# Kernel optimization log

Hardware: AMD Instinct MI355X
Metric: run time of the kernel (lower is better)

## Reference

```python
import jax, jax.numpy as jnp
import numpy as np

N = 50000
E = 600000
IN_DIM = 256
OUT_DIM = 128
SCALE = 1.8
K = 2
ALPHA = 0.15
EPS = 1e-12  # matches F.normalize eps


def setup_inputs() -> dict:
    key = jax.random.key(0)
    k1, k2, k3, k4 = jax.random.split(key, 4)
    x = jax.random.normal(k1, (N, IN_DIM), dtype=jnp.float32)
    edge_index = jax.random.randint(k2, (2, E), 0, N, dtype=jnp.int64)
    # nn.Linear params (Kaiming-uniform-ish init scale)
    lim = 1.0 / np.sqrt(IN_DIM)
    W = jax.random.uniform(k3, (OUT_DIM, IN_DIM), dtype=jnp.float32, minval=-lim, maxval=lim)
    b = jax.random.uniform(k4, (OUT_DIM,), dtype=jnp.float32, minval=-lim, maxval=lim)
    return {"x": x, "edge_index": edge_index, "W": W, "b": b}


def _gcn_norm(edge_index, num_nodes):
    # add self loops, symmetric normalization D^-1/2 A D^-1/2
    loops = jnp.arange(num_nodes, dtype=edge_index.dtype)
    row = jnp.concatenate([edge_index[0], loops])  # source
    col = jnp.concatenate([edge_index[1], loops])  # target
    deg = jax.ops.segment_sum(jnp.ones_like(col, dtype=jnp.float32), col,
                              num_segments=num_nodes)
    dinv = jnp.where(deg > 0, jax.lax.rsqrt(deg), 0.0)
    w = dinv[row] * dinv[col]
    return row, col, w


def reference(x, edge_index, W, b):
    # linear
    h = x @ W.T + b  # [N, OUT_DIM]
    # L2 normalize over feature dim, then scale
    nrm = jnp.sqrt(jnp.sum(h * h, axis=1, keepdims=True))
    h = h / jnp.maximum(nrm, EPS) * SCALE
    # APPNP propagation (eval mode: edge dropout disabled)
    row, col, w = _gcn_norm(edge_index, N)
    z = h
    for _ in range(K):
        msg = w[:, None] * z[row]  # gather + weight, [E+N, OUT_DIM]
        agg = jax.ops.segment_sum(msg, col, num_segments=N)
        z = (1.0 - ALPHA) * agg + ALPHA * h
    return z
```

## Files before the change

### kernel.cpp

```cpp
#include <hip/hip_runtime.h>
#include <hip/hip_bf16.h>

#define NNODES 50000
#define IN_DIM 256
#define OUT_DIM 128
#define SCALE 1.8f
#define ALPHA 0.15f
#define DSTRIDE 64
#define GEMM_BLOCKS 782

typedef unsigned short ushort_t;
typedef __attribute__((ext_vector_type(8))) _Float16 f16x8;
typedef __attribute__((ext_vector_type(4))) float f32x4;


__device__ __forceinline__ unsigned short f2bf_rne(float f) {
    unsigned int u = __float_as_uint(f);
    unsigned int r = u + 0x7fffu + ((u >> 16) & 1u);
    return (unsigned short)(r >> 16);
}

__device__ __forceinline__ float2 bf2_to_f2(unsigned int p) {
    float2 f;
    f.x = __uint_as_float(p << 16);
    f.y = __uint_as_float(p & 0xffff0000u);
    return f;
}

__device__ __forceinline__ unsigned int f2_to_bf2(float x, float y) {
    return (unsigned int)f2bf_rne(x) | ((unsigned int)f2bf_rne(y) << 16);
}

__device__ __forceinline__ unsigned short f2h(float f) {
    _Float16 h = (_Float16)f;
    return *(unsigned short*)&h;
}


#define XPAD 264

__global__ void __launch_bounds__(256, 4) prep_gemm_kernel(
        const float* __restrict__ x, const float* __restrict__ W,
        const float* __restrict__ b,
        const int* __restrict__ row, const int* __restrict__ col, int E,
        int* __restrict__ cnt, ushort_t* __restrict__ csr16,
        ushort_t* __restrict__ u0b) {
    __shared__ __align__(16) ushort_t xh[64][XPAD];

    if (blockIdx.x >= GEMM_BLOCKS) {
        int e0 = ((blockIdx.x - GEMM_BLOCKS) * 256 + threadIdx.x) * 2;
        if (e0 < E) {
            int2 rr = *(const int2*)(row + e0);
            int2 cc = *(const int2*)(col + e0);
            int p0 = atomicAdd(&cnt[cc.x], 1);
            if (p0 < DSTRIDE) csr16[(size_t)cc.x * DSTRIDE + p0] = (ushort_t)rr.x;
            int p1 = atomicAdd(&cnt[cc.y], 1);
            if (p1 < DSTRIDE) csr16[(size_t)cc.y * DSTRIDE + p1] = (ushort_t)rr.y;
        }
        return;
    }

    const int t = threadIdx.x;
    const int wv = t >> 6;
    const int lane = t & 63;
    const int q = lane >> 4;
    const int c = lane & 15;
    const int rowBase = blockIdx.x * 64;

    f16x8 wf[2][8];
    float bias[2];
    #pragma unroll
    for (int j = 0; j < 2; ++j) {
        const size_t base = (size_t)((2 * wv + j) * 16 + c) * IN_DIM + q * 8;
        #pragma unroll
        for (int kt = 0; kt < 8; ++kt) {
            float4 w0 = *(const float4*)(W + base + kt * 32);
            float4 w1 = *(const float4*)(W + base + kt * 32 + 4);
            f16x8 wp;
            wp[0] = (_Float16)w0.x; wp[1] = (_Float16)w0.y;
            wp[2] = (_Float16)w0.z; wp[3] = (_Float16)w0.w;
            wp[4] = (_Float16)w1.x; wp[5] = (_Float16)w1.y;
            wp[6] = (_Float16)w1.z; wp[7] = (_Float16)w1.w;
            wf[j][kt] = wp;
        }
        bias[j] = b[(2 * wv + j) * 16 + c];
    }

    #pragma unroll
    for (int it = 0; it < 16; ++it) {
        int s = it * 256 + t;
        int r = s >> 6;
        int ks = (s & 63) * 4;
        int grow = rowBase + r;
        float4 v = make_float4(0.f, 0.f, 0.f, 0.f);
        if (grow < NNODES) v = *(const float4*)(x + (size_t)grow * IN_DIM + ks);
        uint2 p;
        p.x = (unsigned int)f2h(v.x) | ((unsigned int)f2h(v.y) << 16);
        p.y = (unsigned int)f2h(v.z) | ((unsigned int)f2h(v.w) << 16);
        *(uint2*)&xh[r][ks] = p;
    }
    __syncthreads();

    f32x4 acc[4][2];
    #pragma unroll
    for (int m = 0; m < 4; ++m)
        #pragma unroll
        for (int j = 0; j < 2; ++j) {
            acc[m][j][0] = bias[j]; acc[m][j][1] = bias[j];
            acc[m][j][2] = bias[j]; acc[m][j][3] = bias[j];
        }

    #pragma unroll
    for (int kt = 0; kt < 8; ++kt) {
        const int kb = kt * 32 + q * 8;
        #pragma unroll
        for (int m = 0; m < 4; ++m) {
            f16x8 a = *(const f16x8*)&xh[m * 16 + c][kb];
            #pragma unroll
            for (int j = 0; j < 2; ++j)
                acc[m][j] = __builtin_amdgcn_mfma_f32_16x16x32_f16(a, wf[j][kt], acc[m][j], 0, 0, 0);
        }
    }

    float psum[4][4];
    #pragma unroll
    for (int m = 0; m < 4; ++m)
        #pragma unroll
        for (int r = 0; r < 4; ++r)
            psum[m][r] = acc[m][0][r] * acc[m][0][r] + acc[m][1][r] * acc[m][1][r];
    #pragma unroll
    for (int mask = 1; mask < 16; mask <<= 1)
        #pragma unroll
        for (int m = 0; m < 4; ++m)
            #pragma unroll
            for (int r = 0; r < 4; ++r)
                psum[m][r] += __shfl_xor(psum[m][r], mask);

    __syncthreads();
    float* red = (float*)&xh[0][0];
    float* scl = red + 64 * 8;
    if (c == 0) {
        #pragma unroll
        for (int m = 0; m < 4; ++m)
            #pragma unroll
            for (int r = 0; r < 4; ++r)
                red[(m * 16 + q * 4 + r) * 8 + wv] = psum[m][r];
    }
    __syncthreads();
    if (t < 64) {
        float s = red[t * 8 + 0] + red[t * 8 + 1] + red[t * 8 + 2] + red[t * 8 + 3];
        scl[t] = SCALE / fmaxf(sqrtf(s), 1e-12f);
    }
    __syncthreads();

    #pragma unroll
    for (int m = 0; m < 4; ++m) {
        #pragma unroll
        for (int r = 0; r < 4; ++r) {
            int lrow = m * 16 + q * 4 + r;
            int grow = rowBase + lrow;
            if (grow < NNODES) {
                float sc = scl[lrow];
                #pragma unroll
                for (int j = 0; j < 2; ++j) {
                    float o = acc[m][j][r] * sc;
                    u0b[(size_t)grow * OUT_DIM + (2 * wv + j) * 16 + c] = f2bf_rne(o);
                }
            }
        }
    }
}


template <int FINAL>
__global__ void __launch_bounds__(256) gather_kernel(
        const int* __restrict__ cnt, const ushort_t* __restrict__ csr16,
        const unsigned int* __restrict__ sin, const unsigned int* __restrict__ u0,
        unsigned int* __restrict__ sout_b, float* __restrict__ out_f) {
    const int wv = threadIdx.x >> 6;
    const int lane = threadIdx.x & 63;
    const int qd = lane >> 4;
    const int d16 = lane & 15;
    const int c = blockIdx.x * 4 + wv;

    const int deg = cnt[c];
    int n = deg;
    if (n > DSTRIDE) n = DSTRIDE;
    int idx = 0;
    if (lane < n) idx = (int)csr16[(size_t)c * DSTRIDE + lane];

    float2 a[4];
    #pragma unroll
    for (int k = 0; k < 4; ++k) a[k] = make_float2(0.f, 0.f);

    int j = 0;
    for (; j + 8 <= n; j += 8) {
        int r0 = __shfl(idx, j + qd);
        int r1 = __shfl(idx, j + 4 + qd);
        float sc0 = 1.0f, sc1 = 1.0f;
        if (!FINAL) {
            sc0 = rsqrtf((float)(cnt[r0] + 1));
            sc1 = rsqrtf((float)(cnt[r1] + 1));
        }
        uint4 v0 = *(const uint4*)(sin + (size_t)r0 * 64 + d16 * 4);
        uint4 v1 = *(const uint4*)(sin + (size_t)r1 * 64 + d16 * 4);
        {
            float2 f0 = bf2_to_f2(v0.x), f1 = bf2_to_f2(v0.y);
            float2 f2 = bf2_to_f2(v0.z), f3 = bf2_to_f2(v0.w);
            a[0].x += sc0 * f0.x; a[0].y += sc0 * f0.y;
            a[1].x += sc0 * f1.x; a[1].y += sc0 * f1.y;
            a[2].x += sc0 * f2.x; a[2].y += sc0 * f2.y;
            a[3].x += sc0 * f3.x; a[3].y += sc0 * f3.y;
        }
        {
            float2 f0 = bf2_to_f2(v1.x), f1 = bf2_to_f2(v1.y);
            float2 f2 = bf2_to_f2(v1.z), f3 = bf2_to_f2(v1.w);
            a[0].x += sc1 * f0.x; a[0].y += sc1 * f0.y;
            a[1].x += sc1 * f1.x; a[1].y += sc1 * f1.y;
            a[2].x += sc1 * f2.x; a[2].y += sc1 * f2.y;
            a[3].x += sc1 * f3.x; a[3].y += sc1 * f3.y;
        }
    }
    for (; j < n; j += 4) {
        int jj = j + qd;
        int rr = __shfl(idx, (jj < n) ? jj : (n - 1));
        if (jj < n) {
            float sc = 1.0f;
            if (!FINAL) sc = rsqrtf((float)(cnt[rr] + 1));
            uint4 v = *(const uint4*)(sin + (size_t)rr * 64 + d16 * 4);
            float2 f0 = bf2_to_f2(v.x), f1 = bf2_to_f2(v.y);
            float2 f2 = bf2_to_f2(v.z), f3 = bf2_to_f2(v.w);
            a[0].x += sc * f0.x; a[0].y += sc * f0.y;
            a[1].x += sc * f1.x; a[1].y += sc * f1.y;
            a[2].x += sc * f2.x; a[2].y += sc * f2.y;
            a[3].x += sc * f3.x; a[3].y += sc * f3.y;
        }
    }

    #pragma unroll
    for (int k = 0; k < 4; ++k) {
        a[k].x += __shfl_xor(a[k].x, 16);
        a[k].y += __shfl_xor(a[k].y, 16);
        a[k].x += __shfl_xor(a[k].x, 32);
        a[k].y += __shfl_xor(a[k].y, 32);
    }

    if (qd == 0) {
        const float degp1 = (float)(deg + 1);
        const float dc = rsqrtf(degp1);
        uint4 zc4 = *(const uint4*)(sin + (size_t)c * 64 + d16 * 4);
        float2 zc[4];
        zc[0] = bf2_to_f2(zc4.x); zc[1] = bf2_to_f2(zc4.y);
        zc[2] = bf2_to_f2(zc4.z); zc[3] = bf2_to_f2(zc4.w);
        if (FINAL) {
            #pragma unroll
            for (int k = 0; k < 4; ++k) {
                a[k].x += zc[k].x;
                a[k].y += zc[k].y;
            }
            uint4 z04 = *(const uint4*)(u0 + (size_t)c * 64 + d16 * 4);
            float2 z0[4];
            z0[0] = bf2_to_f2(z04.x); z0[1] = bf2_to_f2(z04.y);
            z0[2] = bf2_to_f2(z04.z); z0[3] = bf2_to_f2(z04.w);
            float gx = (1.0f - ALPHA) * dc;
            float4 o0, o1;
            o0.x = gx * a[0].x + ALPHA * z0[0].x;
            o0.y = gx * a[0].y + ALPHA * z0[0].y;
            o0.z = gx * a[1].x + ALPHA * z0[1].x;
            o0.w = gx * a[1].y + ALPHA * z0[1].y;
            o1.x = gx * a[2].x + ALPHA * z0[2].x;
            o1.y = gx * a[2].y + ALPHA * z0[2].y;
            o1.z = gx * a[3].x + ALPHA * z0[3].x;
            o1.w = gx * a[3].y + ALPHA * z0[3].y;
            float* p = out_f + (size_t)c * 128 + d16 * 8;
            *(float4*)(p) = o0;
            *(float4*)(p + 4) = o1;
        } else {
            #pragma unroll
            for (int k = 0; k < 4; ++k) {
                a[k].x += dc * zc[k].x;
                a[k].y += dc * zc[k].y;
            }
            float qc = (1.0f - ALPHA) * dc * dc;
            float ac = ALPHA * dc;
            uint4 w;
            w.x = f2_to_bf2(qc * a[0].x + ac * zc[0].x, qc * a[0].y + ac * zc[0].y);
            w.y = f2_to_bf2(qc * a[1].x + ac * zc[1].x, qc * a[1].y + ac * zc[1].y);
            w.z = f2_to_bf2(qc * a[2].x + ac * zc[2].x, qc * a[2].y + ac * zc[2].y);
            w.w = f2_to_bf2(qc * a[3].x + ac * zc[3].x, qc * a[3].y + ac * zc[3].y);
            *(uint4*)(sout_b + (size_t)c * 64 + d16 * 4) = w;
        }
    }
}

extern "C" void kernel_launch(void* const* d_in, const int* in_sizes, int n_in,
                              void* d_out, int out_size, void* d_ws, size_t ws_size,
                              hipStream_t stream) {
    const float* x  = (const float*)d_in[0];
    const int*   ei = (const int*)d_in[1];
    const float* W  = (const float*)d_in[2];
    const float* b  = (const float*)d_in[3];
    float* out = (float*)d_out;

    int E = in_sizes[1] / 2;
    const int* row = ei;
    const int* col = ei + E;

    unsigned int* u0b = (unsigned int*)d_ws;
    unsigned int* s1b = u0b + (size_t)NNODES * 64;
    int* cnt = (int*)(s1b + (size_t)NNODES * 64);
    ushort_t* csr16 = (ushort_t*)(cnt + 50048);

    hipMemsetAsync(cnt, 0, 50048 * sizeof(int), stream);

    int fillBlocks = (E + 511) / 512;
    prep_gemm_kernel<<<GEMM_BLOCKS + fillBlocks, 256, 0, stream>>>(
        x, W, b, row, col, E, cnt, csr16, (ushort_t*)u0b);

    gather_kernel<0><<<NNODES / 4, 256, 0, stream>>>(cnt, csr16, u0b, u0b, s1b, nullptr);
    gather_kernel<1><<<NNODES / 4, 256, 0, stream>>>(cnt, csr16, s1b, u0b, nullptr, out);
}
```

Baseline: 198.6 us.

## Load x directly into MFMA registers with 32-row GEMM tiles, dropping LDS staging

The fused prep/GEMM kernel no longer stages x through a 64x264 fp16 shared-memory tile. Each lane now loads its own x fragments from global memory, converts them to fp16 and feeds them straight into the MFMAs. The tile height drops from 64 to 32 rows, so the block count doubles and occupancy is no longer pinned by LDS, and the fill-block count is hardcoded for E. The intent is to remove the LDS round trip and its barrier and to raise parallelism. The cost is strided, less coalesced global loads of x and the W fragments being reloaded in twice as many blocks.

```diff
diff --git a/kernel.cpp b/kernel.cpp
--- a/kernel.cpp
+++ b/kernel.cpp
@@ -7,7 +7,8 @@
 #define SCALE 1.8f
 #define ALPHA 0.15f
 #define DSTRIDE 64
-#define GEMM_BLOCKS 782
+#define GEMM_BLOCKS 1563
+#define FILL_BLOCKS 1172
 
 typedef unsigned short ushort_t;
 typedef __attribute__((ext_vector_type(8))) _Float16 f16x8;
@@ -21,31 +22,26 @@
 }
 
 __device__ __forceinline__ float2 bf2_to_f2(unsigned int p) {
-    float2 f;
-    f.x = __uint_as_float(p << 16);
-    f.y = __uint_as_float(p & 0xffff0000u);
-    return f;
+    float f;
+    float2 o;
+    o.x = __uint_as_float(p << 16);
+    o.y = __uint_as_float(p & 0xffff0000u);
+    (void)f;
+    return o;
 }
 
 __device__ __forceinline__ unsigned int f2_to_bf2(float x, float y) {
     return (unsigned int)f2bf_rne(x) | ((unsigned int)f2bf_rne(y) << 16);
 }
 
-__device__ __forceinline__ unsigned short f2h(float f) {
-    _Float16 h = (_Float16)f;
-    return *(unsigned short*)&h;
-}
-
-
-#define XPAD 264
-
-__global__ void __launch_bounds__(256, 4) prep_gemm_kernel(
+
+__global__ void __launch_bounds__(256) prep_gemm_kernel(
         const float* __restrict__ x, const float* __restrict__ W,
         const float* __restrict__ b,
         const int* __restrict__ row, const int* __restrict__ col, int E,
         int* __restrict__ cnt, ushort_t* __restrict__ csr16,
         ushort_t* __restrict__ u0b) {
-    __shared__ __align__(16) ushort_t xh[64][XPAD];
+    __shared__ float red[32 * 8 + 32];
 
     if (blockIdx.x >= GEMM_BLOCKS) {
         int e0 = ((blockIdx.x - GEMM_BLOCKS) * 256 + threadIdx.x) * 2;
@@ -65,7 +61,7 @@
     const int lane = t & 63;
     const int q = lane >> 4;
     const int c = lane & 15;
-    const int rowBase = blockIdx.x * 64;
+    const int rowBase = blockIdx.x * 32;
 
     f16x8 wf[2][8];
     float bias[2];
@@ -86,24 +82,9 @@
         bias[j] = b[(2 * wv + j) * 16 + c];
     }
 
-    #pragma unroll
-    for (int it = 0; it < 16; ++it) {
-        int s = it * 256 + t;
-        int r = s >> 6;
-        int ks = (s & 63) * 4;
-        int grow = rowBase + r;
-        float4 v = make_float4(0.f, 0.f, 0.f, 0.f);
-        if (grow < NNODES) v = *(const float4*)(x + (size_t)grow * IN_DIM + ks);
-        uint2 p;
-        p.x = (unsigned int)f2h(v.x) | ((unsigned int)f2h(v.y) << 16);
-        p.y = (unsigned int)f2h(v.z) | ((unsigned int)f2h(v.w) << 16);
-        *(uint2*)&xh[r][ks] = p;
-    }
-    __syncthreads();
-
-    f32x4 acc[4][2];
-    #pragma unroll
-    for (int m = 0; m < 4; ++m)
+    f32x4 acc[2][2];
+    #pragma unroll
+    for (int m = 0; m < 2; ++m)
         #pragma unroll
         for (int j = 0; j < 2; ++j) {
             acc[m][j][0] = bias[j]; acc[m][j][1] = bias[j];
@@ -111,50 +92,60 @@
         }
 
     #pragma unroll
-    for (int kt = 0; kt < 8; ++kt) {
-        const int kb = kt * 32 + q * 8;
-        #pragma unroll
-        for (int m = 0; m < 4; ++m) {
-            f16x8 a = *(const f16x8*)&xh[m * 16 + c][kb];
+    for (int m = 0; m < 2; ++m) {
+        const int grow = rowBase + m * 16 + c;
+        const bool ok = (grow < NNODES);
+        const float* rowp = x + (size_t)grow * IN_DIM + q * 8;
+        #pragma unroll
+        for (int kt = 0; kt < 8; ++kt) {
+            float4 xa = make_float4(0.f, 0.f, 0.f, 0.f);
+            float4 xb = make_float4(0.f, 0.f, 0.f, 0.f);
+            if (ok) {
+                xa = *(const float4*)(rowp + kt * 32);
+                xb = *(const float4*)(rowp + kt * 32 + 4);
+            }
+            f16x8 a;
+            a[0] = (_Float16)xa.x; a[1] = (_Float16)xa.y;
+            a[2] = (_Float16)xa.z; a[3] = (_Float16)xa.w;
+            a[4] = (_Float16)xb.x; a[5] = (_Float16)xb.y;
+            a[6] = (_Float16)xb.z; a[7] = (_Float16)xb.w;
             #pragma unroll
             for (int j = 0; j < 2; ++j)
                 acc[m][j] = __builtin_amdgcn_mfma_f32_16x16x32_f16(a, wf[j][kt], acc[m][j], 0, 0, 0);
         }
     }
 
-    float psum[4][4];
-    #pragma unroll
-    for (int m = 0; m < 4; ++m)
+    float psum[2][4];
+    #pragma unroll
+    for (int m = 0; m < 2; ++m)
         #pragma unroll
         for (int r = 0; r < 4; ++r)
             psum[m][r] = acc[m][0][r] * acc[m][0][r] + acc[m][1][r] * acc[m][1][r];
     #pragma unroll
     for (int mask = 1; mask < 16; mask <<= 1)
         #pragma unroll
-        for (int m = 0; m < 4; ++m)
+        for (int m = 0; m < 2; ++m)
             #pragma unroll
             for (int r = 0; r < 4; ++r)
                 psum[m][r] += __shfl_xor(psum[m][r], mask);
 
-    __syncthreads();
-    float* red = (float*)&xh[0][0];
-    float* scl = red + 64 * 8;
+    float* scl = red + 32 * 8;
     if (c == 0) {
         #pragma unroll
-        for (int m = 0; m < 4; ++m)
+        for (int m = 0; m < 2; ++m)
             #pragma unroll
             for (int r = 0; r < 4; ++r)
                 red[(m * 16 + q * 4 + r) * 8 + wv] = psum[m][r];
     }
     __syncthreads();
-    if (t < 64) {
+    if (t < 32) {
         float s = red[t * 8 + 0] + red[t * 8 + 1] + red[t * 8 + 2] + red[t * 8 + 3];
         scl[t] = SCALE / fmaxf(sqrtf(s), 1e-12f);
     }
     __syncthreads();
 
     #pragma unroll
-    for (int m = 0; m < 4; ++m) {
+    for (int m = 0; m < 2; ++m) {
         #pragma unroll
         for (int r = 0; r < 4; ++r) {
             int lrow = m * 16 + q * 4 + r;
@@ -313,8 +304,7 @@
 
     hipMemsetAsync(cnt, 0, 50048 * sizeof(int), stream);
 
-    int fillBlocks = (E + 511) / 512;
-    prep_gemm_kernel<<<GEMM_BLOCKS + fillBlocks, 256, 0, stream>>>(
+    prep_gemm_kernel<<<GEMM_BLOCKS + FILL_BLOCKS, 256, 0, stream>>>(
         x, W, b, row, col, E, cnt, csr16, (ushort_t*)u0b);
 
     gather_kernel<0><<<NNODES / 4, 256, 0, stream>>>(cnt, csr16, u0b, u0b, s1b, nullptr);
```

After: 209.7 us. +5.6%, slower.
